# Performance work log

Measured on AMD Instinct MI355X. Metric: run time of the kernel, lower is better.

Reference implementation:

```python
import jax, jax.numpy as jnp
import numpy as np

N = 50000   # nodes
E = 800000  # edges
D = 64      # num_filters == hidden_channels
NG = 5      # num_gaussians (edge_attr width, unused by forward math)
NEG_SLOPE = 0.2


def setup_inputs() -> dict:
    key = jax.random.key(0)
    ks = jax.random.split(key, 16)
    s = 1.0 / np.sqrt(D)
    return {
        "x": jax.random.normal(ks[0], (N, D), dtype=jnp.float32),
        "edge_index": jax.random.randint(ks[1], (2, E), 0, N, dtype=jnp.int64),
        "edge_weight": jax.random.uniform(ks[2], (E,), dtype=jnp.float32),
        "edge_attr": jax.random.normal(ks[3], (E, NG), dtype=jnp.float32),
        "W0": jax.random.normal(ks[4], (D, D), dtype=jnp.float32) * s,
        "b0": jnp.zeros((D,), dtype=jnp.float32),
        "W1": jax.random.normal(ks[5], (D, D), dtype=jnp.float32) * s,
        "as1": jax.random.normal(ks[6], (D,), dtype=jnp.float32) * s,
        "ad1": jax.random.normal(ks[7], (D,), dtype=jnp.float32) * s,
        "b1": jnp.zeros((D,), dtype=jnp.float32),
        "W2": jax.random.normal(ks[8], (D, D), dtype=jnp.float32) * s,
        "as2": jax.random.normal(ks[9], (D,), dtype=jnp.float32) * s,
        "ad2": jax.random.normal(ks[10], (D,), dtype=jnp.float32) * s,
        "b2": jnp.zeros((D,), dtype=jnp.float32),
    }


def gat_layer(h, src, dst, W, a_src, a_dst, b):
    # PyG GATConv, heads=1, add_self_loops=False
    hx = h @ W  # [N, D]
    # per-node attention logits, gathered per edge (edge j->i: src=j, dst=i)
    alpha = (hx * a_src).sum(-1)[src] + (hx * a_dst).sum(-1)[dst]  # [E]
    alpha = jax.nn.leaky_relu(alpha, NEG_SLOPE)
    # segment softmax grouped by destination node
    m = jax.ops.segment_max(alpha, dst, num_segments=N)
    e = jnp.exp(alpha - m[dst])
    s = jax.ops.segment_sum(e, dst, num_segments=N)
    p = e / s[dst]  # [E]
    # scatter-add weighted source features
    out = jax.ops.segment_sum(hx[src] * p[:, None], dst, num_segments=N)
    return out + b


def reference(x, edge_index, edge_weight, edge_attr,
              W0, b0, W1, as1, ad1, b1, W2, as2, ad2, b2):
    # edge_weight / edge_attr are accepted but unused, as in the torch module
    src, dst = edge_index[0], edge_index[1]
    out = jax.nn.relu(x @ W0 + b0)
    out = out + jax.nn.relu(gat_layer(out, src, dst, W1, as1, ad1, b1))
    out = out + jax.nn.relu(gat_layer(out, src, dst, W2, as2, ad2, b2))
    return out
```

## Files before the change

### kernel.cpp

```cpp
#include <hip/hip_runtime.h>

#define DD 64
#define NEG_SLOPE 0.2f
#define HS 68
#define CAP 64
#define BSH 8
#define BN  256
#define NBMAX 256
#define NBLK 256
#define STAGE_CAP 6144
#define AMM_NODES 32

__device__ __forceinline__ unsigned short f2bf(float f)
{
    unsigned u = __float_as_uint(f);
    u += 0x7FFFu + ((u >> 16) & 1u);
    return (unsigned short)(u >> 16);
}
__device__ __forceinline__ float bf2f(unsigned short b)
{
    return __uint_as_float(((unsigned)b) << 16);
}

__device__ __forceinline__ int wave_incl_scan(int v, int lane)
{
#pragma unroll
    for (int off = 1; off < 64; off <<= 1) {
        int t = __shfl_up(v, off);
        if (lane >= off) v += t;
    }
    return v;
}

__global__ __launch_bounds__(512) void count_mm(
    const int4* __restrict__ dst4, const int* __restrict__ dst,
    int* __restrict__ cnts, int NB, int E4, int E, int C4,
    const float* __restrict__ x, const float* __restrict__ W0,
    const float* __restrict__ b0, const float* __restrict__ W1,
    const float* __restrict__ a_src, const float* __restrict__ a_dst,
    float* __restrict__ h, ushort4* __restrict__ hxb4,
    float* __restrict__ sarr, float* __restrict__ darr, int n)
{
    __shared__ float smem[DD * DD + DD * HS];
    int tid = threadIdx.x;

    if (blockIdx.x < NBLK) {
        int* lh = (int*)smem;
        int k = blockIdx.x;
        for (int i = tid; i < NB; i += 512) lh[i] = 0;
        __syncthreads();
        int i0 = k * C4, i1 = min(i0 + C4, E4);
        for (int i = i0 + tid; i < i1; i += 512) {
            int4 d = dst4[i];
            atomicAdd(&lh[d.x >> BSH], 1);
            atomicAdd(&lh[d.y >> BSH], 1);
            atomicAdd(&lh[d.z >> BSH], 1);
            atomicAdd(&lh[d.w >> BSH], 1);
        }
        if (k == NBLK - 1) {
            for (int e = E4 * 4 + tid; e < E; e += 512)
                atomicAdd(&lh[dst[e] >> BSH], 1);
        }
        __syncthreads();
        for (int i = tid; i < NB; i += 512) cnts[k * NB + i] = lh[i];
        return;
    }

    float* Wsh = smem;
    float* Hsh = smem + DD * DD;
    int fg = tid & 15, ng = tid >> 4;
    int tile0 = (blockIdx.x - NBLK) * 64;

    for (int i = tid * 4; i < DD * DD; i += 2048)
        *(float4*)&Wsh[i] = *(const float4*)&W0[i];
    for (int p = 0; p < 2; ++p) {
        int nl = p * 32 + ng, gn = tile0 + nl;
        if (gn < n)
            *(float4*)&Hsh[nl * HS + 4 * fg] = *(const float4*)&x[gn * DD + 4 * fg];
    }
    __syncthreads();

    float4 acc[2];
#pragma unroll
    for (int j = 0; j < 2; ++j) acc[j] = float4{0.f, 0.f, 0.f, 0.f};
#pragma unroll 8
    for (int k = 0; k < DD; ++k) {
        float4 w4 = *(float4*)&Wsh[k * DD + 4 * fg];
#pragma unroll
        for (int j = 0; j < 2; ++j) {
            float hv = Hsh[(2 * ng + j) * HS + k];
            acc[j].x += hv * w4.x; acc[j].y += hv * w4.y;
            acc[j].z += hv * w4.z; acc[j].w += hv * w4.w;
        }
    }

    float4 b4 = *(const float4*)&b0[4 * fg];
    float4 o[2];
#pragma unroll
    for (int j = 0; j < 2; ++j) {
        o[j].x = fmaxf(acc[j].x + b4.x, 0.f);
        o[j].y = fmaxf(acc[j].y + b4.y, 0.f);
        o[j].z = fmaxf(acc[j].z + b4.z, 0.f);
        o[j].w = fmaxf(acc[j].w + b4.w, 0.f);
        int gn = tile0 + 2 * ng + j;
        if (gn < n) *(float4*)&h[gn * DD + 4 * fg] = o[j];
    }
    __syncthreads();

#pragma unroll
    for (int j = 0; j < 2; ++j)
        *(float4*)&Hsh[(2 * ng + j) * HS + 4 * fg] = o[j];
    for (int i = tid * 4; i < DD * DD; i += 2048)
        *(float4*)&Wsh[i] = *(const float4*)&W1[i];
    __syncthreads();

#pragma unroll
    for (int j = 0; j < 2; ++j) acc[j] = float4{0.f, 0.f, 0.f, 0.f};
#pragma unroll 8
    for (int k = 0; k < DD; ++k) {
        float4 w4 = *(float4*)&Wsh[k * DD + 4 * fg];
#pragma unroll
        for (int j = 0; j < 2; ++j) {
            float hv = Hsh[(2 * ng + j) * HS + k];
            acc[j].x += hv * w4.x; acc[j].y += hv * w4.y;
            acc[j].z += hv * w4.z; acc[j].w += hv * w4.w;
        }
    }

    float4 as4 = *(const float4*)&a_src[4 * fg];
    float4 ad4 = *(const float4*)&a_dst[4 * fg];
#pragma unroll
    for (int j = 0; j < 2; ++j) {
        int gn = tile0 + 2 * ng + j;
        if (gn < n) {
            ushort4 hb;
            hb.x = f2bf(acc[j].x); hb.y = f2bf(acc[j].y);
            hb.z = f2bf(acc[j].z); hb.w = f2bf(acc[j].w);
            hxb4[gn * 16 + fg] = hb;
        }
        float ps = acc[j].x * as4.x + acc[j].y * as4.y + acc[j].z * as4.z + acc[j].w * as4.w;
        float pd = acc[j].x * ad4.x + acc[j].y * ad4.y + acc[j].z * ad4.z + acc[j].w * ad4.w;
#pragma unroll
        for (int off = 8; off; off >>= 1) {
            ps += __shfl_xor(ps, off);
            pd += __shfl_xor(pd, off);
        }
        if (fg == 0 && gn < n) { sarr[gn] = ps; darr[gn] = pd; }
    }
}

__global__ __launch_bounds__(1024) void csr_scan(
    const int* __restrict__ cnts, int* __restrict__ boff, int* __restrict__ cbase,
    int* __restrict__ row_ptr, int NB, int N, int E)
{
    __shared__ int psum[16][NBMAX];
    __shared__ int tot[NBMAX];
    __shared__ int sbo[NBMAX];
    __shared__ int wsum[4];
    int tid = threadIdx.x, lane = tid & 63, w = tid >> 6;

#pragma unroll
    for (int b0 = 0; b0 < NBMAX; b0 += 64) {
        int b = b0 + lane;
        int s = 0;
        if (b < NB) {
            int k0 = 16 * w;
#pragma unroll
            for (int k = 0; k < 16; ++k) s += cnts[(k0 + k) * NB + b];
        }
        psum[w][b] = s;
    }
    __syncthreads();

    if (tid < NBMAX) {
        int run = 0;
#pragma unroll
        for (int w2 = 0; w2 < 16; ++w2) {
            int c = psum[w2][tid];
            psum[w2][tid] = run;
            run += c;
        }
        tot[tid] = run;
    }
    __syncthreads();

    if (tid < 256) {
        int v = (tid < NB) ? tot[tid] : 0;
        int incl = wave_incl_scan(v, lane);
        if (lane == 63) wsum[w] = incl;
        __syncthreads();
        int wo = 0;
        for (int i = 0; i < w; ++i) wo += wsum[i];
        int excl = wo + incl - v;
        sbo[tid] = excl;
        if (tid < NB) boff[tid] = excl;
    } else {
        __syncthreads();
    }
    if (tid == 0) { boff[NB] = E; row_ptr[N] = E; }
    __syncthreads();

#pragma unroll
    for (int b0 = 0; b0 < NBMAX; b0 += 64) {
        int b = b0 + lane;
        if (b < NB) {
            int run = sbo[b] + psum[w][b];
            int k0 = 16 * w;
#pragma unroll
            for (int k = 0; k < 16; ++k) {
                int c = cnts[(k0 + k) * NB + b];
                cbase[(k0 + k) * NB + b] = run;
                run += c;
            }
        }
    }
}

__global__ __launch_bounds__(512) void chunk_scatter(
    const int4* __restrict__ dst4, const int4* __restrict__ src4,
    const int* __restrict__ dst, const int* __restrict__ src,
    const int* __restrict__ cbase, int* __restrict__ ebuf,
    int NB, int E4, int E, int C4)
{
    __shared__ int lcur[NBMAX];
    int k = blockIdx.x, tid = threadIdx.x;
    for (int i = tid; i < NB; i += 512) lcur[i] = cbase[k * NB + i];
    __syncthreads();
    int i0 = k * C4, i1 = min(i0 + C4, E4);
    for (int i = i0 + tid; i < i1; i += 512) {
        int4 d = dst4[i];
        int4 s = src4[i];
        int b, p;
        b = d.x >> BSH; p = atomicAdd(&lcur[b], 1); ebuf[p] = ((d.x & (BN - 1)) << 24) | s.x;
        b = d.y >> BSH; p = atomicAdd(&lcur[b], 1); ebuf[p] = ((d.y & (BN - 1)) << 24) | s.y;
        b = d.z >> BSH; p = atomicAdd(&lcur[b], 1); ebuf[p] = ((d.z & (BN - 1)) << 24) | s.z;
        b = d.w >> BSH; p = atomicAdd(&lcur[b], 1); ebuf[p] = ((d.w & (BN - 1)) << 24) | s.w;
    }
    if (k == NBLK - 1) {
        for (int e = E4 * 4 + tid; e < E; e += 512) {
            int d = dst[e];
            int b = d >> BSH;
            int p = atomicAdd(&lcur[b], 1);
            ebuf[p] = ((d & (BN - 1)) << 24) | src[e];
        }
    }
}

__global__ __launch_bounds__(512) void group_build(
    const int* __restrict__ ebuf, const int* __restrict__ boff,
    int* __restrict__ row_ptr, int* __restrict__ col, int N)
{
    __shared__ int lcnt[BN];
    __shared__ int loff[BN];
    __shared__ int lcur[BN];
    __shared__ int wsum[4];
    __shared__ int stage[STAGE_CAP];
    int b = blockIdx.x, tid = threadIdx.x;
    int e0 = boff[b], e1 = boff[b + 1];
    int total = e1 - e0;
    if (tid < BN) { lcnt[tid] = 0; lcur[tid] = 0; }
    __syncthreads();
    for (int e = e0 + tid; e < e1; e += 512)
        atomicAdd(&lcnt[((unsigned)ebuf[e]) >> 24], 1);
    __syncthreads();
    int lane = tid & 63, w = tid >> 6;
    int v = (tid < BN) ? lcnt[tid] : 0;
    int incl = wave_incl_scan(v, lane);
    if (tid < BN && lane == 63) wsum[w] = incl;
    __syncthreads();
    if (tid < BN) {
        int wo = 0;
        for (int i = 0; i < w; ++i) wo += wsum[i];
        int excl = wo + incl - v;
        loff[tid] = excl;
        int node = b * BN + tid;
        if (node < N) row_ptr[node] = e0 + excl;
    }
    __syncthreads();
    if (total <= STAGE_CAP) {
        for (int e = e0 + tid; e < e1; e += 512) {
            int p = ebuf[e];
            int dl = ((unsigned)p) >> 24;
            int r = atomicAdd(&lcur[dl], 1);
            stage[loff[dl] + r] = p & 0xFFFFFF;
        }
        __syncthreads();
        for (int i = tid; i < total; i += 512)
            col[e0 + i] = stage[i];
    } else {
        for (int e = e0 + tid; e < e1; e += 512) {
            int p = ebuf[e];
            int dl = ((unsigned)p) >> 24;
            int r = atomicAdd(&lcur[dl], 1);
            col[e0 + loff[dl] + r] = p & 0xFFFFFF;
        }
    }
}

__global__ __launch_bounds__(512) void agg_mm(
    const ushort4* __restrict__ hxA, const int* __restrict__ row_ptr,
    const int* __restrict__ col, const float* __restrict__ sA,
    const float* __restrict__ dA, const float* __restrict__ bias,
    float* __restrict__ h, const float* __restrict__ W,
    const float* __restrict__ a_src, const float* __restrict__ a_dst,
    ushort4* __restrict__ hxB, float* __restrict__ sB, float* __restrict__ dB,
    int n)
{
    __shared__ float Wsh[DD * DD];
    __shared__ float Hsh[AMM_NODES * HS];
    __shared__ float aw[8][CAP];
    __shared__ int   ac[8][CAP];
    int tid = threadIdx.x;
    int w = tid >> 6, lane = tid & 63, fg = lane & 15, es = lane >> 4;
    int tile0 = blockIdx.x * AMM_NODES;

    for (int i = tid * 4; i < DD * DD; i += 2048)
        *(float4*)&Wsh[i] = *(const float4*)&W[i];

    for (int q = 0; q < 4; ++q) {
        int nl = 4 * w + q;
        int v = tile0 + nl;
        if (v >= n) continue;

        int beg = row_ptr[v], end = row_ptr[v + 1];
        int deg = end - beg;
        float adi = dA[v];
        float m = -3.4e38f, s = 0.f;
        float4 acc = float4{0.f, 0.f, 0.f, 0.f};

        if (deg <= CAP) {
            for (int e = beg + lane; e < end; e += 64) {
                int c = col[e];
                float a = sA[c] + adi;
                a = a > 0.f ? a : NEG_SLOPE * a;
                ac[w][e - beg] = c;
                aw[w][e - beg] = a;
                m = fmaxf(m, a);
            }
#pragma unroll
            for (int off = 32; off; off >>= 1) m = fmaxf(m, __shfl_xor(m, off));
            for (int i = lane; i < deg; i += 64) {
                float wv = __expf(aw[w][i] - m);
                aw[w][i] = wv; s += wv;
            }
#pragma unroll
            for (int off = 32; off; off >>= 1) s += __shfl_xor(s, off);
#pragma unroll 2
            for (int i = es; i < deg; i += 4) {
                int c = ac[w][i];
                float wv = aw[w][i];
                ushort4 u = hxA[c * 16 + fg];
                acc.x += wv * bf2f(u.x); acc.y += wv * bf2f(u.y);
                acc.z += wv * bf2f(u.z); acc.w += wv * bf2f(u.w);
            }
        } else {
            for (int e = beg + lane; e < end; e += 64) {
                float a = sA[col[e]] + adi;
                a = a > 0.f ? a : NEG_SLOPE * a;
                m = fmaxf(m, a);
            }
#pragma unroll
            for (int off = 32; off; off >>= 1) m = fmaxf(m, __shfl_xor(m, off));
            for (int e = beg + lane; e < end; e += 64) {
                float a = sA[col[e]] + adi;
                a = a > 0.f ? a : NEG_SLOPE * a;
                s += __expf(a - m);
            }
#pragma unroll
            for (int off = 32; off; off >>= 1) s += __shfl_xor(s, off);
            for (int e = beg + es; e < end; e += 4) {
                int c = col[e];
                float a = sA[c] + adi;
                a = a > 0.f ? a : NEG_SLOPE * a;
                float wv = __expf(a - m);
                ushort4 u = hxA[c * 16 + fg];
                acc.x += wv * bf2f(u.x); acc.y += wv * bf2f(u.y);
                acc.z += wv * bf2f(u.z); acc.w += wv * bf2f(u.w);
            }
        }

        acc.x += __shfl_xor(acc.x, 16); acc.y += __shfl_xor(acc.y, 16);
        acc.z += __shfl_xor(acc.z, 16); acc.w += __shfl_xor(acc.w, 16);
        acc.x += __shfl_xor(acc.x, 32); acc.y += __shfl_xor(acc.y, 32);
        acc.z += __shfl_xor(acc.z, 32); acc.w += __shfl_xor(acc.w, 32);

        if (es == 0) {
            float inv = (s > 0.f) ? 1.f / s : 0.f;
            float4 b4 = ((const float4*)bias)[fg];
            float4 o;
            o.x = fmaxf(acc.x * inv + b4.x, 0.f);
            o.y = fmaxf(acc.y * inv + b4.y, 0.f);
            o.z = fmaxf(acc.z * inv + b4.z, 0.f);
            o.w = fmaxf(acc.w * inv + b4.w, 0.f);
            float4* hp = (float4*)&h[v * DD + 4 * fg];
            float4 cur = *hp;
            cur.x += o.x; cur.y += o.y; cur.z += o.z; cur.w += o.w;
            *hp = cur;
            *(float4*)&Hsh[nl * HS + 4 * fg] = cur;
        }
    }
    __syncthreads();

    int nl2 = tid >> 4;
    float4 acc2 = float4{0.f, 0.f, 0.f, 0.f};
#pragma unroll 8
    for (int k = 0; k < DD; ++k) {
        float4 w4 = *(float4*)&Wsh[k * DD + 4 * fg];
        float hv = Hsh[nl2 * HS + k];
        acc2.x += hv * w4.x; acc2.y += hv * w4.y;
        acc2.z += hv * w4.z; acc2.w += hv * w4.w;
    }
    int gn = tile0 + nl2;
    float4 as4 = *(const float4*)&a_src[4 * fg];
    float4 ad4 = *(const float4*)&a_dst[4 * fg];
    if (gn < n) {
        ushort4 hb;
        hb.x = f2bf(acc2.x); hb.y = f2bf(acc2.y);
        hb.z = f2bf(acc2.z); hb.w = f2bf(acc2.w);
        hxB[gn * 16 + fg] = hb;
    }
    float ps = acc2.x * as4.x + acc2.y * as4.y + acc2.z * as4.z + acc2.w * as4.w;
    float pd = acc2.x * ad4.x + acc2.y * ad4.y + acc2.z * ad4.z + acc2.w * ad4.w;
#pragma unroll
    for (int off = 8; off; off >>= 1) {
        ps += __shfl_xor(ps, off);
        pd += __shfl_xor(pd, off);
    }
    if (fg == 0 && gn < n) { sB[gn] = ps; dB[gn] = pd; }
}

__global__ __launch_bounds__(256) void aggregate(
    const ushort4* __restrict__ hxb4, const int* __restrict__ row_ptr,
    const int* __restrict__ col, const float* __restrict__ sarr,
    const float* __restrict__ darr, const float* __restrict__ bias,
    float* __restrict__ h, int n)
{
    __shared__ float aw[4][CAP];
    __shared__ int   ac[4][CAP];
    int tid = threadIdx.x;
    int wid = tid >> 6, lane = tid & 63, fg = lane & 15, es = lane >> 4;
    int v = blockIdx.x * 4 + wid;
    if (v >= n) return;

    int beg = row_ptr[v], end = row_ptr[v + 1];
    int deg = end - beg;
    float adi = darr[v];
    float m = -3.4e38f, s = 0.f;
    float4 acc = float4{0.f, 0.f, 0.f, 0.f};

    if (deg <= CAP) {
        for (int e = beg + lane; e < end; e += 64) {
            int c = col[e];
            float a = sarr[c] + adi;
            a = a > 0.f ? a : NEG_SLOPE * a;
            ac[wid][e - beg] = c;
            aw[wid][e - beg] = a;
            m = fmaxf(m, a);
        }
#pragma unroll
        for (int off = 32; off; off >>= 1) m = fmaxf(m, __shfl_xor(m, off));
        for (int i = lane; i < deg; i += 64) {
            float w = __expf(aw[wid][i] - m);
            aw[wid][i] = w; s += w;
        }
#pragma unroll
        for (int off = 32; off; off >>= 1) s += __shfl_xor(s, off);
#pragma unroll 2
        for (int i = es; i < deg; i += 4) {
            int c = ac[wid][i];
            float w = aw[wid][i];
            ushort4 u = hxb4[c * 16 + fg];
            acc.x += w * bf2f(u.x); acc.y += w * bf2f(u.y);
            acc.z += w * bf2f(u.z); acc.w += w * bf2f(u.w);
        }
    } else {
        for (int e = beg + lane; e < end; e += 64) {
            float a = sarr[col[e]] + adi;
            a = a > 0.f ? a : NEG_SLOPE * a;
            m = fmaxf(m, a);
        }
#pragma unroll
        for (int off = 32; off; off >>= 1) m = fmaxf(m, __shfl_xor(m, off));
        for (int e = beg + lane; e < end; e += 64) {
            float a = sarr[col[e]] + adi;
            a = a > 0.f ? a : NEG_SLOPE * a;
            s += __expf(a - m);
        }
#pragma unroll
        for (int off = 32; off; off >>= 1) s += __shfl_xor(s, off);
        for (int e = beg + es; e < end; e += 4) {
            int c = col[e];
            float a = sarr[c] + adi;
            a = a > 0.f ? a : NEG_SLOPE * a;
            float w = __expf(a - m);
            ushort4 u = hxb4[c * 16 + fg];
            acc.x += w * bf2f(u.x); acc.y += w * bf2f(u.y);
            acc.z += w * bf2f(u.z); acc.w += w * bf2f(u.w);
        }
    }

    acc.x += __shfl_xor(acc.x, 16); acc.y += __shfl_xor(acc.y, 16);
    acc.z += __shfl_xor(acc.z, 16); acc.w += __shfl_xor(acc.w, 16);
    acc.x += __shfl_xor(acc.x, 32); acc.y += __shfl_xor(acc.y, 32);
    acc.z += __shfl_xor(acc.z, 32); acc.w += __shfl_xor(acc.w, 32);

    if (es == 0) {
        float inv = (s > 0.f) ? 1.f / s : 0.f;
        float4 b4 = ((const float4*)bias)[fg];
        float4 o;
        o.x = fmaxf(acc.x * inv + b4.x, 0.f);
        o.y = fmaxf(acc.y * inv + b4.y, 0.f);
        o.z = fmaxf(acc.z * inv + b4.z, 0.f);
        o.w = fmaxf(acc.w * inv + b4.w, 0.f);
        float4* hp = (float4*)&h[v * DD + 4 * fg];
        float4 cur = *hp;
        cur.x += o.x; cur.y += o.y; cur.z += o.z; cur.w += o.w;
        *hp = cur;
    }
}

extern "C" void kernel_launch(void* const* d_in, const int* in_sizes, int n_in,
                              void* d_out, int out_size, void* d_ws, size_t ws_size,
                              hipStream_t stream)
{
    const float* x  = (const float*)d_in[0];
    const int*   ei = (const int*)d_in[1];
    const float* W0 = (const float*)d_in[4];
    const float* b0 = (const float*)d_in[5];
    const float* W1 = (const float*)d_in[6];
    const float* as1= (const float*)d_in[7];
    const float* ad1= (const float*)d_in[8];
    const float* b1 = (const float*)d_in[9];
    const float* W2 = (const float*)d_in[10];
    const float* as2= (const float*)d_in[11];
    const float* ad2= (const float*)d_in[12];
    const float* b2 = (const float*)d_in[13];

    int N = in_sizes[0] / DD;
    int E = in_sizes[1] / 2;
    int E4 = E >> 2;
    int C4 = (E4 + NBLK - 1) / NBLK;
    int NB = (N + BN - 1) >> BSH;
    float* h = (float*)d_out;

    ushort4* hxA  = (ushort4*)d_ws;
    ushort4* hxB  = hxA + (size_t)N * 16;
    float* sA     = (float*)(hxB + (size_t)N * 16);
    float* dA     = sA + N;
    float* sB     = dA + N;
    float* dB     = sB + N;
    int*   row_ptr= (int*)(dB + N);
    int*   cnts   = row_ptr + (N + 1);
    int*   cbase  = cnts + NBLK * NB;
    int*   boff   = cbase + NBLK * NB;
    int*   ebuf   = boff + (NB + 1);
    int*   colb   = ebuf + E;

    const int* src = ei;
    const int* dst = ei + E;
    const int4* dst4 = (const int4*)dst;
    const int4* src4 = (const int4*)src;

    int mm_tiles  = (N + 63) / 64;
    int amm_blks  = (N + AMM_NODES - 1) / AMM_NODES;
    int agg_blks  = (N + 3) / 4;

    count_mm<<<NBLK + mm_tiles, 512, 0, stream>>>(
        dst4, dst, cnts, NB, E4, E, C4,
        x, W0, b0, W1, as1, ad1, h, hxA, sA, dA, N);
    csr_scan<<<1, 1024, 0, stream>>>(cnts, boff, cbase, row_ptr, NB, N, E);
    chunk_scatter<<<NBLK, 512, 0, stream>>>(dst4, src4, dst, src, cbase, ebuf, NB, E4, E, C4);
    group_build<<<NB, 512, 0, stream>>>(ebuf, boff, row_ptr, colb, N);
    agg_mm<<<amm_blks, 512, 0, stream>>>(hxA, row_ptr, colb, sA, dA, b1,
                                         h, W2, as2, ad2, hxB, sB, dB, N);
    aggregate<<<agg_blks, 256, 0, stream>>>(hxB, row_ptr, colb, sB, dB, b2, h, N);
}
```

Measured before the change: 204.8 us.

## Assign one 16-lane group per node in GAT aggregation kernels

Both aggregation kernels now use a 16-lane group per destination node instead of a full wave per node. Each group holds up to 64 edge logits in registers, reduces max and sum with 16-lane shuffles, and stages (col, weight) pairs in a per-group shared buffer. The gather then walks all edges with each lane owning 4 features, so the cross-subgroup accumulator reduction is gone. agg_mm reuses that buffer as the H tile behind an extra barrier. The standalone aggregate kernel moves to 512-thread blocks of 32 nodes. The aim is better lane utilisation for average degree about 16 and fewer shuffles, at the cost of longer serial gather chains per lane.

New measurement: 194.4 us. -5.1%, faster.

```diff
diff --git a/kernel.cpp b/kernel.cpp
--- a/kernel.cpp
+++ b/kernel.cpp
@@ -10,6 +10,7 @@
 #define NBLK 256
 #define STAGE_CAP 6144
 #define AMM_NODES 32
+#define CWS 65
 
 __device__ __forceinline__ unsigned short f2bf(float f)
 {
@@ -30,6 +31,83 @@
         if (lane >= off) v += t;
     }
     return v;
+}
+
+__device__ __forceinline__ void group_aggregate(
+    const ushort4* __restrict__ hx, const int* __restrict__ col,
+    const float* __restrict__ sarr, float adi, int beg, int deg, int fl,
+    uint2* __restrict__ cw, float4& acc, float& s)
+{
+    float m = -3.4e38f;
+    s = 0.f;
+    acc = float4{0.f, 0.f, 0.f, 0.f};
+
+    if (deg <= CAP) {
+        int c0 = 0, c1 = 0, c2 = 0, c3 = 0;
+        float a0 = 0.f, a1 = 0.f, a2 = 0.f, a3 = 0.f;
+        if (fl < deg)      { c0 = col[beg + fl];      float a = sarr[c0] + adi; a0 = a > 0.f ? a : NEG_SLOPE * a; m = fmaxf(m, a0); }
+        if (fl + 16 < deg) { c1 = col[beg + fl + 16]; float a = sarr[c1] + adi; a1 = a > 0.f ? a : NEG_SLOPE * a; m = fmaxf(m, a1); }
+        if (fl + 32 < deg) { c2 = col[beg + fl + 32]; float a = sarr[c2] + adi; a2 = a > 0.f ? a : NEG_SLOPE * a; m = fmaxf(m, a2); }
+        if (fl + 48 < deg) { c3 = col[beg + fl + 48]; float a = sarr[c3] + adi; a3 = a > 0.f ? a : NEG_SLOPE * a; m = fmaxf(m, a3); }
+#pragma unroll
+        for (int off = 8; off; off >>= 1) m = fmaxf(m, __shfl_xor(m, off));
+        float w0 = 0.f, w1 = 0.f, w2 = 0.f, w3 = 0.f;
+        if (fl < deg)      { w0 = __expf(a0 - m); s += w0; }
+        if (fl + 16 < deg) { w1 = __expf(a1 - m); s += w1; }
+        if (fl + 32 < deg) { w2 = __expf(a2 - m); s += w2; }
+        if (fl + 48 < deg) { w3 = __expf(a3 - m); s += w3; }
+#pragma unroll
+        for (int off = 8; off; off >>= 1) s += __shfl_xor(s, off);
+
+        int degR = (deg + 3) & ~3;
+        if (fl < degR)      { uint2 e; e.x = (unsigned)c0; e.y = __float_as_uint(w0); cw[fl] = e; }
+        if (fl + 16 < degR) { uint2 e; e.x = (unsigned)c1; e.y = __float_as_uint(w1); cw[fl + 16] = e; }
+        if (fl + 32 < degR) { uint2 e; e.x = (unsigned)c2; e.y = __float_as_uint(w2); cw[fl + 32] = e; }
+        if (fl + 48 < degR) { uint2 e; e.x = (unsigned)c3; e.y = __float_as_uint(w3); cw[fl + 48] = e; }
+
+#define GATH(P) { float wv = __uint_as_float((P).y);                          \
+                  ushort4 uu = hx[(P).x * 16 + fl];                           \
+                  acc.x += wv * bf2f(uu.x); acc.y += wv * bf2f(uu.y);         \
+                  acc.z += wv * bf2f(uu.z); acc.w += wv * bf2f(uu.w); }
+        for (int i = 0; i < degR; i += 4) {
+            uint2 p0 = cw[i], p1 = cw[i + 1], p2 = cw[i + 2], p3 = cw[i + 3];
+            GATH(p0); GATH(p1); GATH(p2); GATH(p3);
+        }
+    } else {
+        for (int i = fl; i < deg; i += 16) {
+            int c = col[beg + i];
+            float a = sarr[c] + adi;
+            a = a > 0.f ? a : NEG_SLOPE * a;
+            m = fmaxf(m, a);
+        }
+#pragma unroll
+        for (int off = 8; off; off >>= 1) m = fmaxf(m, __shfl_xor(m, off));
+        for (int i = fl; i < deg; i += 16) {
+            int c = col[beg + i];
+            float a = sarr[c] + adi;
+            a = a > 0.f ? a : NEG_SLOPE * a;
+            s += __expf(a - m);
+        }
+#pragma unroll
+        for (int off = 8; off; off >>= 1) s += __shfl_xor(s, off);
+        for (int base = 0; base < deg; base += 16) {
+            int i = base + fl;
+            uint2 e; e.x = 0u; e.y = 0u;
+            if (i < deg) {
+                int c = col[beg + i];
+                float a = sarr[c] + adi;
+                a = a > 0.f ? a : NEG_SLOPE * a;
+                e.x = (unsigned)c; e.y = __float_as_uint(__expf(a - m));
+            }
+            cw[fl] = e;
+#pragma unroll
+            for (int j = 0; j < 16; j += 4) {
+                uint2 p0 = cw[j], p1 = cw[j + 1], p2 = cw[j + 2], p3 = cw[j + 3];
+                GATH(p0); GATH(p1); GATH(p2); GATH(p3);
+            }
+        }
+    }
+#undef GATH
 }
 
 __global__ __launch_bounds__(512) void count_mm(
@@ -307,101 +385,53 @@
     int n)
 {
     __shared__ float Wsh[DD * DD];
-    __shared__ float Hsh[AMM_NODES * HS];
-    __shared__ float aw[8][CAP];
-    __shared__ int   ac[8][CAP];
+    __shared__ uint2 cwbuf[AMM_NODES][CWS];
+    float* Hsh = (float*)&cwbuf[0][0];
+
     int tid = threadIdx.x;
-    int w = tid >> 6, lane = tid & 63, fg = lane & 15, es = lane >> 4;
+    int w = tid >> 6, lane = tid & 63, grp = lane >> 4, fl = lane & 15;
+    int nl = 4 * w + grp;
     int tile0 = blockIdx.x * AMM_NODES;
+    int v = tile0 + nl;
+    bool alive = v < n;
 
     for (int i = tid * 4; i < DD * DD; i += 2048)
         *(float4*)&Wsh[i] = *(const float4*)&W[i];
 
-    for (int q = 0; q < 4; ++q) {
-        int nl = 4 * w + q;
-        int v = tile0 + nl;
-        if (v >= n) continue;
-
-        int beg = row_ptr[v], end = row_ptr[v + 1];
-        int deg = end - beg;
-        float adi = dA[v];
-        float m = -3.4e38f, s = 0.f;
-        float4 acc = float4{0.f, 0.f, 0.f, 0.f};
-
-        if (deg <= CAP) {
-            for (int e = beg + lane; e < end; e += 64) {
-                int c = col[e];
-                float a = sA[c] + adi;
-                a = a > 0.f ? a : NEG_SLOPE * a;
-                ac[w][e - beg] = c;
-                aw[w][e - beg] = a;
-                m = fmaxf(m, a);
-            }
-#pragma unroll
-            for (int off = 32; off; off >>= 1) m = fmaxf(m, __shfl_xor(m, off));
-            for (int i = lane; i < deg; i += 64) {
-                float wv = __expf(aw[w][i] - m);
-                aw[w][i] = wv; s += wv;
-            }
-#pragma unroll
-            for (int off = 32; off; off >>= 1) s += __shfl_xor(s, off);
-#pragma unroll 2
-            for (int i = es; i < deg; i += 4) {
-                int c = ac[w][i];
-                float wv = aw[w][i];
-                ushort4 u = hxA[c * 16 + fg];
-                acc.x += wv * bf2f(u.x); acc.y += wv * bf2f(u.y);
-                acc.z += wv * bf2f(u.z); acc.w += wv * bf2f(u.w);
-            }
-        } else {
-            for (int e = beg + lane; e < end; e += 64) {
-                float a = sA[col[e]] + adi;
-                a = a > 0.f ? a : NEG_SLOPE * a;
-                m = fmaxf(m, a);
-            }
-#pragma unroll
-            for (int off = 32; off; off >>= 1) m = fmaxf(m, __shfl_xor(m, off));
-            for (int e = beg + lane; e < end; e += 64) {
-                float a = sA[col[e]] + adi;
-                a = a > 0.f ? a : NEG_SLOPE * a;
-                s += __expf(a - m);
-            }
-#pragma unroll
-            for (int off = 32; off; off >>= 1) s += __shfl_xor(s, off);
-            for (int e = beg + es; e < end; e += 4) {
-                int c = col[e];
-                float a = sA[c] + adi;
-                a = a > 0.f ? a : NEG_SLOPE * a;
-                float wv = __expf(a - m);
-                ushort4 u = hxA[c * 16 + fg];
-                acc.x += wv * bf2f(u.x); acc.y += wv * bf2f(u.y);
-                acc.z += wv * bf2f(u.z); acc.w += wv * bf2f(u.w);
-            }
-        }
-
-        acc.x += __shfl_xor(acc.x, 16); acc.y += __shfl_xor(acc.y, 16);
-        acc.z += __shfl_xor(acc.z, 16); acc.w += __shfl_xor(acc.w, 16);
-        acc.x += __shfl_xor(acc.x, 32); acc.y += __shfl_xor(acc.y, 32);
-        acc.z += __shfl_xor(acc.z, 32); acc.w += __shfl_xor(acc.w, 32);
-
-        if (es == 0) {
-            float inv = (s > 0.f) ? 1.f / s : 0.f;
-            float4 b4 = ((const float4*)bias)[fg];
-            float4 o;
-            o.x = fmaxf(acc.x * inv + b4.x, 0.f);
-            o.y = fmaxf(acc.y * inv + b4.y, 0.f);
-            o.z = fmaxf(acc.z * inv + b4.z, 0.f);
-            o.w = fmaxf(acc.w * inv + b4.w, 0.f);
-            float4* hp = (float4*)&h[v * DD + 4 * fg];
+    int beg = 0, deg = 0;
+    float adi = 0.f;
+    if (alive) {
+        beg = row_ptr[v];
+        deg = row_ptr[v + 1] - beg;
+        adi = dA[v];
+    }
+
+    float4 acc; float s;
+    group_aggregate(hxA, col, sA, adi, beg, deg, fl, &cwbuf[nl][0], acc, s);
+
+    float4 resid = float4{0.f, 0.f, 0.f, 0.f};
+    {
+        float inv = (s > 0.f) ? 1.f / s : 0.f;
+        float4 b4 = ((const float4*)bias)[fl];
+        float4 o;
+        o.x = fmaxf(acc.x * inv + b4.x, 0.f);
+        o.y = fmaxf(acc.y * inv + b4.y, 0.f);
+        o.z = fmaxf(acc.z * inv + b4.z, 0.f);
+        o.w = fmaxf(acc.w * inv + b4.w, 0.f);
+        if (alive) {
+            float4* hp = (float4*)&h[v * DD + 4 * fl];
             float4 cur = *hp;
             cur.x += o.x; cur.y += o.y; cur.z += o.z; cur.w += o.w;
             *hp = cur;
-            *(float4*)&Hsh[nl * HS + 4 * fg] = cur;
-        }
-    }
+            resid = cur;
+        }
+    }
+    __syncthreads();
+    *(float4*)&Hsh[nl * HS + 4 * fl] = resid;
     __syncthreads();
 
     int nl2 = tid >> 4;
+    int fg = tid & 15;
     float4 acc2 = float4{0.f, 0.f, 0.f, 0.f};
 #pragma unroll 8
     for (int k = 0; k < DD; ++k) {
@@ -429,90 +459,39 @@
     if (fg == 0 && gn < n) { sB[gn] = ps; dB[gn] = pd; }
 }
 
-__global__ __launch_bounds__(256) void aggregate(
+__global__ __launch_bounds__(512) void aggregate(
     const ushort4* __restrict__ hxb4, const int* __restrict__ row_ptr,
     const int* __restrict__ col, const float* __restrict__ sarr,
     const float* __restrict__ darr, const float* __restrict__ bias,
     float* __restrict__ h, int n)
 {
-    __shared__ float aw[4][CAP];
-    __shared__ int   ac[4][CAP];
+    __shared__ uint2 cwbuf[AMM_NODES][CWS];
     int tid = threadIdx.x;
-    int wid = tid >> 6, lane = tid & 63, fg = lane & 15, es = lane >> 4;
-    int v = blockIdx.x * 4 + wid;
-    if (v >= n) return;
-
-    int beg = row_ptr[v], end = row_ptr[v + 1];
-    int deg = end - beg;
-    float adi = darr[v];
-    float m = -3.4e38f, s = 0.f;
-    float4 acc = float4{0.f, 0.f, 0.f, 0.f};
-
-    if (deg <= CAP) {
-        for (int e = beg + lane; e < end; e += 64) {
-            int c = col[e];
-            float a = sarr[c] + adi;
-            a = a > 0.f ? a : NEG_SLOPE * a;
-            ac[wid][e - beg] = c;
-            aw[wid][e - beg] = a;
-            m = fmaxf(m, a);
-        }
-#pragma unroll
-        for (int off = 32; off; off >>= 1) m = fmaxf(m, __shfl_xor(m, off));
-        for (int i = lane; i < deg; i += 64) {
-            float w = __expf(aw[wid][i] - m);
-            aw[wid][i] = w; s += w;
-        }
-#pragma unroll
-        for (int off = 32; off; off >>= 1) s += __shfl_xor(s, off);
-#pragma unroll 2
-        for (int i = es; i < deg; i += 4) {
-            int c = ac[wid][i];
-            float w = aw[wid][i];
-            ushort4 u = hxb4[c * 16 + fg];
-            acc.x += w * bf2f(u.x); acc.y += w * bf2f(u.y);
-            acc.z += w * bf2f(u.z); acc.w += w * bf2f(u.w);
-        }
-    } else {
-        for (int e = beg + lane; e < end; e += 64) {
-            float a = sarr[col[e]] + adi;
-            a = a > 0.f ? a : NEG_SLOPE * a;
-            m = fmaxf(m, a);
-        }
-#pragma unroll
-        for (int off = 32; off; off >>= 1) m = fmaxf(m, __shfl_xor(m, off));
-        for (int e = beg + lane; e < end; e += 64) {
-            float a = sarr[col[e]] + adi;
-            a = a > 0.f ? a : NEG_SLOPE * a;
-            s += __expf(a - m);
-        }
-#pragma unroll
-        for (int off = 32; off; off >>= 1) s += __shfl_xor(s, off);
-        for (int e = beg + es; e < end; e += 4) {
-            int c = col[e];
-            float a = sarr[c] + adi;
-            a = a > 0.f ? a : NEG_SLOPE * a;
-            float w = __expf(a - m);
-            ushort4 u = hxb4[c * 16 + fg];
-            acc.x += w * bf2f(u.x); acc.y += w * bf2f(u.y);
-            acc.z += w * bf2f(u.z); acc.w += w * bf2f(u.w);
-        }
-    }
-
-    acc.x += __shfl_xor(acc.x, 16); acc.y += __shfl_xor(acc.y, 16);
-    acc.z += __shfl_xor(acc.z, 16); acc.w += __shfl_xor(acc.w, 16);
-    acc.x += __shfl_xor(acc.x, 32); acc.y += __shfl_xor(acc.y, 32);
-    acc.z += __shfl_xor(acc.z, 32); acc.w += __shfl_xor(acc.w, 32);
-
-    if (es == 0) {
+    int w = tid >> 6, lane = tid & 63, grp = lane >> 4, fl = lane & 15;
+    int nl = 4 * w + grp;
+    int v = blockIdx.x * AMM_NODES + nl;
+    bool alive = v < n;
+
+    int beg = 0, deg = 0;
+    float adi = 0.f;
+    if (alive) {
+        beg = row_ptr[v];
+        deg = row_ptr[v + 1] - beg;
+        adi = darr[v];
+    }
+
+    float4 acc; float s;
+    group_aggregate(hxb4, col, sarr, adi, beg, deg, fl, &cwbuf[nl][0], acc, s);
+
+    if (alive) {
         float inv = (s > 0.f) ? 1.f / s : 0.f;
-        float4 b4 = ((const float4*)bias)[fg];
+        float4 b4 = ((const float4*)bias)[fl];
         float4 o;
         o.x = fmaxf(acc.x * inv + b4.x, 0.f);
         o.y = fmaxf(acc.y * inv + b4.y, 0.f);
         o.z = fmaxf(acc.z * inv + b4.z, 0.f);
         o.w = fmaxf(acc.w * inv + b4.w, 0.f);
-        float4* hp = (float4*)&h[v * DD + 4 * fg];
+        float4* hp = (float4*)&h[v * DD + 4 * fl];
         float4 cur = *hp;
         cur.x += o.x; cur.y += o.y; cur.z += o.z; cur.w += o.w;
         *hp = cur;
@@ -562,8 +541,7 @@
     const int4* src4 = (const int4*)src;
 
     int mm_tiles  = (N + 63) / 64;
-    int amm_blks  = (N + AMM_NODES - 1) / AMM_NODES;
-    int agg_blks  = (N + 3) / 4;
+    int agg_blks  = (N + AMM_NODES - 1) / AMM_NODES;
 
     count_mm<<<NBLK + mm_tiles, 512, 0, stream>>>(
         dst4, dst, cnts, NB, E4, E, C4,
@@ -571,7 +549,7 @@
     csr_scan<<<1, 1024, 0, stream>>>(cnts, boff, cbase, row_ptr, NB, N, E);
     chunk_scatter<<<NBLK, 512, 0, stream>>>(dst4, src4, dst, src, cbase, ebuf, NB, E4, E, C4);
     group_build<<<NB, 512, 0, stream>>>(ebuf, boff, row_ptr, colb, N);
-    agg_mm<<<amm_blks, 512, 0, stream>>>(hxA, row_ptr, colb, sA, dA, b1,
+    agg_mm<<<agg_blks, 512, 0, stream>>>(hxA, row_ptr, colb, sA, dA, b1,
                                          h, W2, as2, ad2, hxB, sB, dB, N);
-    aggregate<<<agg_blks, 256, 0, stream>>>(hxB, row_ptr, colb, sB, dB, b2, h, N);
-}
+    aggregate<<<agg_blks, 512, 0, stream>>>(hxB, row_ptr, colb, sB, dB, b2, h, N);
+}
```
